# Optimization experiments

Measured on AMD Instinct MI355X. Metric: run time of the kernel, lower is better.

The kernel has to match this reference:

```python
import jax, jax.numpy as jnp
import numpy as np

B, F, D, H = 16384, 39, 16, 2   # batch, fields, embed_dim, heads
VOCAB = 10000                    # per-field vocab
DH = D * H                       # attention output dim per layer (no head split)


def setup_inputs() -> dict:
    key = jax.random.key(0)
    ks = jax.random.split(key, 32)
    def n(k, shape, s=0.05):
        return jax.random.normal(k, shape, jnp.float32) * s
    inp = {"x": jax.random.randint(ks[0], (B, F), 0, VOCAB, dtype=jnp.int32)}
    inp["emb"] = n(ks[1], (F * VOCAB, D))
    idx = 2
    for i, din in enumerate([D, DH, DH]):  # layer0: 16->32, layers 1-2: 32->32
        for nm in ["wq", "wk", "wv", "wr"]:
            inp[f"{nm}{i}"] = n(ks[idx], (din, DH)); idx += 1
    prev = F * DH  # 1248 after flatten
    for i, u in enumerate([128, 64, 32, 1], 1):
        inp[f"w{i}"] = n(ks[idx], (prev, u)); idx += 1
        inp[f"b{i}"] = jnp.zeros((u,), jnp.float32)
        prev = u
    return inp


def reference(x, emb,
              wq0, wk0, wv0, wr0,
              wq1, wk1, wv1, wr1,
              wq2, wk2, wv2, wr2,
              w1, b1, w2, b2, w3, b3, w4, b4):
    offsets = jnp.arange(F, dtype=jnp.int32) * VOCAB
    e = emb[x + offsets]                                   # [B, F, D]
    for wq, wk, wv, wr in [(wq0, wk0, wv0, wr0),
                           (wq1, wk1, wv1, wr1),
                           (wq2, wk2, wv2, wr2)]:
        q = jnp.einsum('bfd,de->bfe', e, wq)               # [B, F, DH]
        k = jnp.einsum('bfd,de->bfe', e, wk)
        v = jnp.einsum('bfd,de->bfe', e, wv)
        att = jax.nn.softmax(jnp.einsum('bfe,bge->bfg', q, k), axis=-1)  # [B,F,F], no scaling
        out = jnp.einsum('bfg,bge->bfe', att, v) + jnp.einsum('bfd,de->bfe', e, wr)
        e = jax.nn.relu(out)
    h = e.reshape(B, F * DH)
    for w, b in [(w1, b1), (w2, b2), (w3, b3)]:
        h = jax.nn.relu(h @ w + b)
    return jax.nn.sigmoid(h @ w4 + b4)                     # [B, 1]
```

## Files before the change

kernel.cpp:

```cpp
#include <hip/hip_runtime.h>
#include <math.h>

#define NF   39
#define NB   16384
#define NVOC 10000

typedef unsigned short u16;
typedef unsigned int   u32;
typedef float f32x4 __attribute__((ext_vector_type(4)));
typedef short s16x8 __attribute__((ext_vector_type(8)));

#define E3_U16   20447232u
#define NSWZ     182272

__device__ __forceinline__ u32 bfadj(float x){
    u32 u = __float_as_uint(x);
    return u + 0x7fffu + ((u >> 16) & 1u);
}
__device__ __forceinline__ u32 pk2(float a, float b){
#if __has_builtin(__builtin_amdgcn_cvt_pk_bf16_f32)
    auto t = __builtin_amdgcn_cvt_pk_bf16_f32(a, b);
    u32 r; __builtin_memcpy(&r, &t, 4); return r;
#else
    return __builtin_amdgcn_perm(bfadj(a), bfadj(b), 0x03020706u);
#endif
}
__device__ __forceinline__ u16 f2bf(float f){ return (u16)(bfadj(f) >> 16); }

__device__ __forceinline__ float fexp2(float x){
#if __has_builtin(__builtin_amdgcn_exp2f)
    return __builtin_amdgcn_exp2f(x);
#else
    return exp2f(x);
#endif
}
__device__ __forceinline__ float frcp(float x){
#if __has_builtin(__builtin_amdgcn_rcpf)
    return __builtin_amdgcn_rcpf(x);
#else
    return 1.f / x;
#endif
}

__device__ __forceinline__ void wave_sync(){
    asm volatile("s_waitcnt lgkmcnt(0)" ::: "memory");
}
__device__ __forceinline__ f32x4 mfma16(s16x8 a, s16x8 b, f32x4 c){
    return __builtin_amdgcn_mfma_f32_16x16x32_bf16(a, b, c, 0, 0, 0);
}
__device__ __forceinline__ void store4(u16* p, f32x4 v){
    *(uint2*)p = make_uint2(pk2(v[0], v[1]), pk2(v[2], v[3]));
}

__global__ void __launch_bounds__(256) swz_kernel(
    const float* __restrict__ wq0, const float* __restrict__ wk0,
    const float* __restrict__ wv0, const float* __restrict__ wr0,
    const float* __restrict__ wq1, const float* __restrict__ wk1,
    const float* __restrict__ wv1, const float* __restrict__ wr1,
    const float* __restrict__ wq2, const float* __restrict__ wk2,
    const float* __restrict__ wv2, const float* __restrict__ wr2,
    const float* __restrict__ w1, const float* __restrict__ w2,
    const float* __restrict__ w3, u16* __restrict__ ws)
{
    int gid = (int)blockIdx.x*256 + (int)threadIdx.x;
    if (gid >= NSWZ) return;
    int w    = gid & 511;
    int lane = w >> 3, j = w & 7;
    int n    = lane & 15, quad = lane >> 4;
    int kin  = quad*8 + j;
    float val;
    if (gid < 12288){
        int mat = gid >> 10;
        int nt  = (gid >> 9) & 1;
        const float* W;
        switch (mat){
            case 0: W = wq0; break; case 1: W = wk0; break;
            case 2: W = wv0; break; case 3: W = wr0; break;
            case 4: W = wq1; break; case 5: W = wk1; break;
            case 6: W = wv1; break; case 7: W = wr1; break;
            case 8: W = wq2; break; case 9: W = wk2; break;
            case 10: W = wv2; break; default: W = wr2; break;
        }
        int din = (mat < 4) ? 16 : 32;
        val = (kin < din) ? W[kin*32 + nt*16 + n] : 0.f;
        if ((mat & 3) == 0) val *= 1.44269504f;
    } else if (gid < 12288 + 159744){
        int tt = (gid - 12288) >> 9;
        int ks = tt >> 3, nt = tt & 7;
        val = w1[(ks*32 + kin)*128 + nt*16 + n];
    } else if (gid < 12288 + 159744 + 8192){
        int tt = (gid - (12288+159744)) >> 9;
        int ks = tt >> 2, nt = tt & 3;
        val = w2[(ks*32 + kin)*64 + nt*16 + n];
    } else {
        int tt = (gid - (12288+159744+8192)) >> 9;
        int ks = tt >> 1, nt = tt & 1;
        val = w3[(ks*32 + kin)*32 + nt*16 + n];
    }
    ws[E3_U16 + gid] = f2bf(val);
}

__global__ void __launch_bounds__(256, 4) attn_kernel(
    const int* __restrict__ x, const float* __restrict__ emb,
    u16* __restrict__ ws)
{
    __shared__ __align__(16) u16 lds[4*5120];
    const int tid  = (int)threadIdx.x;
    const int wid  = tid >> 6, lane = tid & 63;
    const int h    = lane >> 4, nl = lane & 15;
    const int r    = (int)blockIdx.x*4 + wid;

    u16* vBuf = lds + wid*5120;
    u16* eBuf = vBuf;
    u16* kBuf = vBuf + 2048;
    u16* qBuf = kBuf + 1536;
    u16* pBuf = kBuf;
    const u16* wmat = ws + E3_U16;
    const f32x4 z = {0.f, 0.f, 0.f, 0.f};
    const int A_off = nl*8 + (h>>1)*128 + (h&1)*4;

    f32x4 ci;
#pragma unroll
    for (int reg = 0; reg < 4; ++reg)
        ci[reg] = (h*4 + reg >= 7) ? -1e30f : 0.f;

    if (lane < 48){
        int f = lane, mt = f >> 4, fl = f & 15;
        u16* row = eBuf + mt*512 + fl*8;
        if (f < NF){
            const float4* ep = (const float4*)(emb + ((size_t)(x[r*NF + f] + f*NVOC))*16);
            float4 e0 = ep[0], e1 = ep[1], e2 = ep[2], e3 = ep[3];
            *(uint4*)(row)       = make_uint4(pk2(e0.x,e0.y), pk2(e0.z,e0.w),
                                              pk2(e1.x,e1.y), pk2(e1.z,e1.w));
            *(uint4*)(row + 128) = make_uint4(pk2(e2.x,e2.y), pk2(e2.z,e2.w),
                                              pk2(e3.x,e3.y), pk2(e3.z,e3.w));
        } else {
            *(uint4*)(row)       = make_uint4(0,0,0,0);
            *(uint4*)(row + 128) = make_uint4(0,0,0,0);
        }
        *(uint4*)(row + 256) = make_uint4(0,0,0,0);
        *(uint4*)(row + 384) = make_uint4(0,0,0,0);
    }
    wave_sync();

#pragma unroll 1
    for (int L = 0; L < 3; ++L){
        const u16* wB = wmat + L*4096;
        s16x8 bE[3];
#pragma unroll
        for (int nt = 0; nt < 3; ++nt)
            bE[nt] = *(const s16x8*)(eBuf + nt*512 + lane*8);
        wave_sync();

        {
            s16x8 a0 = *(const s16x8*)(wB + lane*8);
            s16x8 a1 = *(const s16x8*)(wB + 512 + lane*8);
#pragma unroll
            for (int nt = 0; nt < 3; ++nt){
                store4(qBuf + nt*512       + A_off, mfma16(a0, bE[nt], z));
                store4(qBuf + nt*512 + 256 + A_off, mfma16(a1, bE[nt], z));
            }
        }
        {
            s16x8 a0 = *(const s16x8*)(wB + 1024 + lane*8);
            s16x8 a1 = *(const s16x8*)(wB + 1536 + lane*8);
#pragma unroll
            for (int nt = 0; nt < 3; ++nt){
                store4(kBuf + nt*512       + A_off, mfma16(a0, bE[nt], z));
                store4(kBuf + nt*512 + 256 + A_off, mfma16(a1, bE[nt], z));
            }
        }
        {
            s16x8 b0 = *(const s16x8*)(wB + 2048 + lane*8);
            s16x8 b1 = *(const s16x8*)(wB + 2560 + lane*8);
#pragma unroll
            for (int mtg = 0; mtg < 3; ++mtg){
                int toff = (mtg>>1)*1024 + (mtg&1)*256;
                store4(vBuf + toff       + A_off, mfma16(bE[mtg], b0, z));
                store4(vBuf + toff + 512 + A_off, mfma16(bE[mtg], b1, z));
            }
            *(uint2*)(vBuf + 2*512 + 256 + lane*4) = make_uint2(0,0);
            *(uint2*)(vBuf + 3*512 + 256 + lane*4) = make_uint2(0,0);
        }
        f32x4 R[2][3];
        {
            s16x8 a0 = *(const s16x8*)(wB + 3072 + lane*8);
            s16x8 a1 = *(const s16x8*)(wB + 3584 + lane*8);
#pragma unroll
            for (int nt = 0; nt < 3; ++nt){
                R[0][nt] = mfma16(a0, bE[nt], z);
                R[1][nt] = mfma16(a1, bE[nt], z);
            }
        }
        wave_sync();

        f32x4 S[3][3];
        {
            s16x8 aK[3], bQ[3];
#pragma unroll
            for (int i = 0; i < 3; ++i){
                aK[i] = *(const s16x8*)(kBuf + i*512 + lane*8);
                bQ[i] = *(const s16x8*)(qBuf + i*512 + lane*8);
            }
#pragma unroll
            for (int mtg = 0; mtg < 3; ++mtg)
#pragma unroll
            for (int nt = 0; nt < 3; ++nt)
                S[mtg][nt] = mfma16(aK[mtg], bQ[nt], (mtg == 2) ? ci : z);
        }
        float inv[3];
#pragma unroll
        for (int nt = 0; nt < 3; ++nt){
            float t = 0.f;
#pragma unroll
            for (int mtg = 0; mtg < 3; ++mtg)
#pragma unroll
            for (int reg = 0; reg < 4; ++reg){
                S[mtg][nt][reg] = fexp2(S[mtg][nt][reg]);
                t += S[mtg][nt][reg];
            }
            t += __shfl_xor(t, 16, 64);
            t += __shfl_xor(t, 32, 64);
            inv[nt] = frcp(t);
        }
#pragma unroll
        for (int mtg = 0; mtg < 3; ++mtg)
#pragma unroll
        for (int nt = 0; nt < 3; ++nt){
            f32x4 p;
#pragma unroll
            for (int reg = 0; reg < 4; ++reg) p[reg] = S[mtg][nt][reg]*inv[nt];
            store4(pBuf + ((mtg>>1)*3 + nt)*512 + (mtg&1)*256 + A_off, p);
        }
        wave_sync();

        s16x8 aV[2][2], bP[2][3];
#pragma unroll
        for (int ks = 0; ks < 2; ++ks){
#pragma unroll
            for (int emt = 0; emt < 2; ++emt)
                aV[ks][emt] = *(const s16x8*)(vBuf + (ks*2+emt)*512 + lane*8);
#pragma unroll
            for (int nt = 0; nt < 3; ++nt)
                bP[ks][nt] = *(const s16x8*)(pBuf + (ks*3+nt)*512 + lane*8);
        }
        wave_sync();
        if (L < 2){
#pragma unroll
            for (int emt = 0; emt < 2; ++emt)
#pragma unroll
            for (int nt = 0; nt < 3; ++nt){
                f32x4 o = mfma16(aV[1][emt], bP[1][nt],
                         mfma16(aV[0][emt], bP[0][nt], R[emt][nt]));
                float m = (nt < 2 || nl < 7) ? 1.f : 0.f;
#pragma unroll
                for (int reg = 0; reg < 4; ++reg)
                    o[reg] = fmaxf(o[reg], 0.f) * m;
                store4(eBuf + nt*512 + emt*256 + A_off, o);
            }
        } else {
            int st = r >> 4, sm = r & 15;
            u32 base = (u32)(st*39)*512u + (u32)(sm*8 + (h>>1)*128 + (h&1)*4);
#pragma unroll
            for (int emt = 0; emt < 2; ++emt)
#pragma unroll
            for (int nt = 0; nt < 3; ++nt){
                f32x4 o = mfma16(aV[1][emt], bP[1][nt],
                         mfma16(aV[0][emt], bP[0][nt], R[emt][nt]));
#pragma unroll
                for (int reg = 0; reg < 4; ++reg)
                    o[reg] = fmaxf(o[reg], 0.f);
                int f = nt*16 + nl;
                if (f < NF)
                    *(uint2*)(ws + base + (u32)f*512u + emt*256) =
                        make_uint2(pk2(o[0], o[1]), pk2(o[2], o[3]));
            }
        }
        wave_sync();
    }
}

__global__ void __launch_bounds__(256, 4) mlp_kernel(
    const float* __restrict__ b1, const float* __restrict__ b2,
    const float* __restrict__ b3, const float* __restrict__ w4,
    const float* __restrict__ b4, const u16* __restrict__ ws,
    float* __restrict__ out)
{
    __shared__ __align__(16) float red[8192];
    __shared__ __align__(16) u16 h1t[2048];
    __shared__ __align__(16) u16 h2t[1024];
    __shared__ float part[32];
    const int tid = (int)threadIdx.x;
    const int w   = tid >> 6, lane = tid & 63;
    const int h   = lane >> 4, nl = lane & 15;
    const int st  = (int)blockIdx.x;
    const int A_off = nl*8 + (h>>1)*128 + (h&1)*4;

    const u16* w1b = ws + E3_U16 + 12288u;
    const u16* w2b = w1b + 159744u;
    const u16* w3b = w2b + 8192u;
    const f32x4 z = {0.f,0.f,0.f,0.f};

    f32x4 acc[8];
#pragma unroll
    for (int nt = 0; nt < 8; ++nt) acc[nt] = z;
#pragma unroll 1
    for (int ks = w; ks < 39; ks += 4){
        s16x8 aE = *(const s16x8*)(ws + (u32)(st*39 + ks)*512u + lane*8);
#pragma unroll
        for (int nt = 0; nt < 8; ++nt){
            s16x8 aW = *(const s16x8*)(w1b + (ks*8 + nt)*512 + lane*8);
            acc[nt] = mfma16(aW, aE, acc[nt]);
        }
    }
#pragma unroll
    for (int nt = 0; nt < 8; ++nt)
        *(f32x4*)(red + (w*8 + nt)*256 + lane*4) = acc[nt];
    __syncthreads();

#pragma unroll
    for (int t = 0; t < 2; ++t){
        int ft = 2*w + t;
        f32x4 s = *(const f32x4*)(red + (0*8 + ft)*256 + lane*4);
#pragma unroll
        for (int p = 1; p < 4; ++p){
            f32x4 q = *(const f32x4*)(red + (p*8 + ft)*256 + lane*4);
#pragma unroll
            for (int reg = 0; reg < 4; ++reg) s[reg] += q[reg];
        }
        float4 bv = *(const float4*)(b1 + ft*16 + h*4);
        f32x4 v;
        v[0] = fmaxf(s[0] + bv.x, 0.f);
        v[1] = fmaxf(s[1] + bv.y, 0.f);
        v[2] = fmaxf(s[2] + bv.z, 0.f);
        v[3] = fmaxf(s[3] + bv.w, 0.f);
        store4(h1t + ft*256 + A_off, v);
    }
    __syncthreads();

    {
        f32x4 a2 = z;
#pragma unroll
        for (int ks = 0; ks < 4; ++ks){
            s16x8 aW = *(const s16x8*)(w2b + (ks*4 + w)*512 + lane*8);
            s16x8 bH = *(const s16x8*)(h1t + ks*512 + lane*8);
            a2 = mfma16(aW, bH, a2);
        }
        float4 bv = *(const float4*)(b2 + w*16 + h*4);
        f32x4 v;
        v[0] = fmaxf(a2[0] + bv.x, 0.f);
        v[1] = fmaxf(a2[1] + bv.y, 0.f);
        v[2] = fmaxf(a2[2] + bv.z, 0.f);
        v[3] = fmaxf(a2[3] + bv.w, 0.f);
        store4(h2t + (w>>1)*512 + (w&1)*256 + A_off, v);
    }
    __syncthreads();

    if (w < 2){
        f32x4 a3 = z;
#pragma unroll
        for (int ks = 0; ks < 2; ++ks){
            s16x8 aW = *(const s16x8*)(w3b + (ks*2 + w)*512 + lane*8);
            s16x8 bH = *(const s16x8*)(h2t + ks*512 + lane*8);
            a3 = mfma16(aW, bH, a3);
        }
        float4 b3v = *(const float4*)(b3 + w*16 + h*4);
        float4 w4v = *(const float4*)(w4 + w*16 + h*4);
        float t = fmaxf(a3[0] + b3v.x, 0.f)*w4v.x
                + fmaxf(a3[1] + b3v.y, 0.f)*w4v.y
                + fmaxf(a3[2] + b3v.z, 0.f)*w4v.z
                + fmaxf(a3[3] + b3v.w, 0.f)*w4v.w;
        t += __shfl_xor(t, 16, 64);
        t += __shfl_xor(t, 32, 64);
        if (h == 0) part[w*16 + nl] = t;
    }
    __syncthreads();
    if (tid < 16){
        float zz = part[tid] + part[16 + tid] + b4[0];
        out[st*16 + tid] = 1.f/(1.f + __expf(-zz));
    }
}

extern "C" void kernel_launch(void* const* d_in, const int* in_sizes, int n_in,
                              void* d_out, int out_size, void* d_ws, size_t ws_size,
                              hipStream_t stream)
{
    (void)in_sizes; (void)n_in; (void)ws_size; (void)out_size;
    const int*   x   = (const int*)d_in[0];
    const float* emb = (const float*)d_in[1];
    u16* ws = (u16*)d_ws;

    swz_kernel<<<(NSWZ+255)/256, 256, 0, stream>>>(
        (const float*)d_in[2],  (const float*)d_in[3],  (const float*)d_in[4],  (const float*)d_in[5],
        (const float*)d_in[6],  (const float*)d_in[7],  (const float*)d_in[8],  (const float*)d_in[9],
        (const float*)d_in[10], (const float*)d_in[11], (const float*)d_in[12], (const float*)d_in[13],
        (const float*)d_in[14], (const float*)d_in[16], (const float*)d_in[18], ws);

    attn_kernel<<<NB/4, 256, 0, stream>>>(x, emb, ws);

    mlp_kernel<<<NB/16, 256, 0, stream>>>(
        (const float*)d_in[15], (const float*)d_in[17], (const float*)d_in[19],
        (const float*)d_in[20], (const float*)d_in[21], ws, (float*)d_out);
}
```

Measured before the change: 189.6 us.

## Process two samples per wave in attention kernel and defer softmax normalization

Each wave now handles two batch rows, sharing the weight fragment loads across both and interleaving their MFMA chains, with the block size reduced to 128 threads. Softmax normalization moves out of the probability store into the output epilogue as a fused multiply-add with the residual, and the residual is no longer seeded into the MFMA accumulator. A redundant per-layer zeroing of the V padding is hoisted into the prologue, and the MLP K loop is unrolled by two. This doubles register pressure per wave, which may lower occupancy.

```diff
diff --git a/kernel.cpp b/kernel.cpp
--- a/kernel.cpp
+++ b/kernel.cpp
@@ -100,21 +100,19 @@
     ws[E3_U16 + gid] = f2bf(val);
 }
 
-__global__ void __launch_bounds__(256, 4) attn_kernel(
+__global__ void __launch_bounds__(128, 2) attn_kernel(
     const int* __restrict__ x, const float* __restrict__ emb,
     u16* __restrict__ ws)
 {
-    __shared__ __align__(16) u16 lds[4*5120];
+    __shared__ __align__(16) u16 lds[2*2*5120];
     const int tid  = (int)threadIdx.x;
     const int wid  = tid >> 6, lane = tid & 63;
     const int h    = lane >> 4, nl = lane & 15;
-    const int r    = (int)blockIdx.x*4 + wid;
-
-    u16* vBuf = lds + wid*5120;
-    u16* eBuf = vBuf;
-    u16* kBuf = vBuf + 2048;
-    u16* qBuf = kBuf + 1536;
-    u16* pBuf = kBuf;
+    const int r0   = (int)blockIdx.x*4 + wid*2;
+
+    u16* base[2];
+    base[0] = lds + wid*10240;
+    base[1] = base[0] + 5120;
     const u16* wmat = ws + E3_U16;
     const f32x4 z = {0.f, 0.f, 0.f, 0.f};
     const int A_off = nl*8 + (h>>1)*128 + (h&1)*4;
@@ -124,78 +122,101 @@
     for (int reg = 0; reg < 4; ++reg)
         ci[reg] = (h*4 + reg >= 7) ? -1e30f : 0.f;
 
-    if (lane < 48){
-        int f = lane, mt = f >> 4, fl = f & 15;
-        u16* row = eBuf + mt*512 + fl*8;
-        if (f < NF){
-            const float4* ep = (const float4*)(emb + ((size_t)(x[r*NF + f] + f*NVOC))*16);
-            float4 e0 = ep[0], e1 = ep[1], e2 = ep[2], e3 = ep[3];
-            *(uint4*)(row)       = make_uint4(pk2(e0.x,e0.y), pk2(e0.z,e0.w),
-                                              pk2(e1.x,e1.y), pk2(e1.z,e1.w));
-            *(uint4*)(row + 128) = make_uint4(pk2(e2.x,e2.y), pk2(e2.z,e2.w),
-                                              pk2(e3.x,e3.y), pk2(e3.z,e3.w));
-        } else {
-            *(uint4*)(row)       = make_uint4(0,0,0,0);
-            *(uint4*)(row + 128) = make_uint4(0,0,0,0);
-        }
-        *(uint4*)(row + 256) = make_uint4(0,0,0,0);
-        *(uint4*)(row + 384) = make_uint4(0,0,0,0);
+#pragma unroll
+    for (int s = 0; s < 2; ++s){
+        u16* eBuf = base[s];
+        if (lane < 48){
+            int f = lane, mt = f >> 4, fl = f & 15;
+            u16* row = eBuf + mt*512 + fl*8;
+            if (f < NF){
+                const float4* ep = (const float4*)(emb + ((size_t)(x[(r0+s)*NF + f] + f*NVOC))*16);
+                float4 e0 = ep[0], e1 = ep[1], e2 = ep[2], e3 = ep[3];
+                *(uint4*)(row)       = make_uint4(pk2(e0.x,e0.y), pk2(e0.z,e0.w),
+                                                  pk2(e1.x,e1.y), pk2(e1.z,e1.w));
+                *(uint4*)(row + 128) = make_uint4(pk2(e2.x,e2.y), pk2(e2.z,e2.w),
+                                                  pk2(e3.x,e3.y), pk2(e3.z,e3.w));
+            } else {
+                *(uint4*)(row)       = make_uint4(0,0,0,0);
+                *(uint4*)(row + 128) = make_uint4(0,0,0,0);
+            }
+            *(uint4*)(row + 256) = make_uint4(0,0,0,0);
+            *(uint4*)(row + 384) = make_uint4(0,0,0,0);
+        }
+        *(uint2*)(base[s] + 3*512 + 256 + lane*4) = make_uint2(0,0);
     }
     wave_sync();
 
 #pragma unroll 1
     for (int L = 0; L < 3; ++L){
         const u16* wB = wmat + L*4096;
-        s16x8 bE[3];
+        s16x8 bE[2][3];
+#pragma unroll
+        for (int s = 0; s < 2; ++s)
 #pragma unroll
         for (int nt = 0; nt < 3; ++nt)
-            bE[nt] = *(const s16x8*)(eBuf + nt*512 + lane*8);
+            bE[s][nt] = *(const s16x8*)(base[s] + nt*512 + lane*8);
         wave_sync();
 
         {
             s16x8 a0 = *(const s16x8*)(wB + lane*8);
             s16x8 a1 = *(const s16x8*)(wB + 512 + lane*8);
 #pragma unroll
-            for (int nt = 0; nt < 3; ++nt){
-                store4(qBuf + nt*512       + A_off, mfma16(a0, bE[nt], z));
-                store4(qBuf + nt*512 + 256 + A_off, mfma16(a1, bE[nt], z));
+            for (int s = 0; s < 2; ++s){
+                u16* qBuf = base[s] + 2048 + 1536;
+#pragma unroll
+                for (int nt = 0; nt < 3; ++nt){
+                    store4(qBuf + nt*512       + A_off, mfma16(a0, bE[s][nt], z));
+                    store4(qBuf + nt*512 + 256 + A_off, mfma16(a1, bE[s][nt], z));
+                }
             }
         }
         {
             s16x8 a0 = *(const s16x8*)(wB + 1024 + lane*8);
             s16x8 a1 = *(const s16x8*)(wB + 1536 + lane*8);
 #pragma unroll
-            for (int nt = 0; nt < 3; ++nt){
-                store4(kBuf + nt*512       + A_off, mfma16(a0, bE[nt], z));
-                store4(kBuf + nt*512 + 256 + A_off, mfma16(a1, bE[nt], z));
+            for (int s = 0; s < 2; ++s){
+                u16* kBuf = base[s] + 2048;
+#pragma unroll
+                for (int nt = 0; nt < 3; ++nt){
+                    store4(kBuf + nt*512       + A_off, mfma16(a0, bE[s][nt], z));
+                    store4(kBuf + nt*512 + 256 + A_off, mfma16(a1, bE[s][nt], z));
+                }
             }
         }
         {
             s16x8 b0 = *(const s16x8*)(wB + 2048 + lane*8);
             s16x8 b1 = *(const s16x8*)(wB + 2560 + lane*8);
 #pragma unroll
-            for (int mtg = 0; mtg < 3; ++mtg){
-                int toff = (mtg>>1)*1024 + (mtg&1)*256;
-                store4(vBuf + toff       + A_off, mfma16(bE[mtg], b0, z));
-                store4(vBuf + toff + 512 + A_off, mfma16(bE[mtg], b1, z));
-            }
-            *(uint2*)(vBuf + 2*512 + 256 + lane*4) = make_uint2(0,0);
-            *(uint2*)(vBuf + 3*512 + 256 + lane*4) = make_uint2(0,0);
-        }
-        f32x4 R[2][3];
+            for (int s = 0; s < 2; ++s){
+                u16* vBuf = base[s];
+#pragma unroll
+                for (int mtg = 0; mtg < 3; ++mtg){
+                    int toff = (mtg>>1)*1024 + (mtg&1)*256;
+                    store4(vBuf + toff       + A_off, mfma16(bE[s][mtg], b0, z));
+                    store4(vBuf + toff + 512 + A_off, mfma16(bE[s][mtg], b1, z));
+                }
+                *(uint2*)(vBuf + 2*512 + 256 + lane*4) = make_uint2(0,0);
+            }
+        }
+        f32x4 R[2][2][3];
         {
             s16x8 a0 = *(const s16x8*)(wB + 3072 + lane*8);
             s16x8 a1 = *(const s16x8*)(wB + 3584 + lane*8);
 #pragma unroll
+            for (int s = 0; s < 2; ++s)
+#pragma unroll
             for (int nt = 0; nt < 3; ++nt){
-                R[0][nt] = mfma16(a0, bE[nt], z);
-                R[1][nt] = mfma16(a1, bE[nt], z);
+                R[s][0][nt] = mfma16(a0, bE[s][nt], z);
+                R[s][1][nt] = mfma16(a1, bE[s][nt], z);
             }
         }
         wave_sync();
 
-        f32x4 S[3][3];
-        {
+        f32x4 S[2][3][3];
+#pragma unroll
+        for (int s = 0; s < 2; ++s){
+            u16* kBuf = base[s] + 2048;
+            u16* qBuf = kBuf + 1536;
             s16x8 aK[3], bQ[3];
 #pragma unroll
             for (int i = 0; i < 3; ++i){
@@ -206,9 +227,11 @@
             for (int mtg = 0; mtg < 3; ++mtg)
 #pragma unroll
             for (int nt = 0; nt < 3; ++nt)
-                S[mtg][nt] = mfma16(aK[mtg], bQ[nt], (mtg == 2) ? ci : z);
-        }
-        float inv[3];
+                S[s][mtg][nt] = mfma16(aK[mtg], bQ[nt], (mtg == 2) ? ci : z);
+        }
+        float inv[2][3];
+#pragma unroll
+        for (int s = 0; s < 2; ++s)
 #pragma unroll
         for (int nt = 0; nt < 3; ++nt){
             float t = 0.f;
@@ -216,64 +239,71 @@
             for (int mtg = 0; mtg < 3; ++mtg)
 #pragma unroll
             for (int reg = 0; reg < 4; ++reg){
-                S[mtg][nt][reg] = fexp2(S[mtg][nt][reg]);
-                t += S[mtg][nt][reg];
+                S[s][mtg][nt][reg] = fexp2(S[s][mtg][nt][reg]);
+                t += S[s][mtg][nt][reg];
             }
             t += __shfl_xor(t, 16, 64);
             t += __shfl_xor(t, 32, 64);
-            inv[nt] = frcp(t);
-        }
-#pragma unroll
-        for (int mtg = 0; mtg < 3; ++mtg)
-#pragma unroll
-        for (int nt = 0; nt < 3; ++nt){
-            f32x4 p;
-#pragma unroll
-            for (int reg = 0; reg < 4; ++reg) p[reg] = S[mtg][nt][reg]*inv[nt];
-            store4(pBuf + ((mtg>>1)*3 + nt)*512 + (mtg&1)*256 + A_off, p);
+            inv[s][nt] = frcp(t);
+        }
+#pragma unroll
+        for (int s = 0; s < 2; ++s){
+            u16* pBuf = base[s] + 2048;
+#pragma unroll
+            for (int mtg = 0; mtg < 3; ++mtg)
+#pragma unroll
+            for (int nt = 0; nt < 3; ++nt)
+                store4(pBuf + ((mtg>>1)*3 + nt)*512 + (mtg&1)*256 + A_off,
+                       S[s][mtg][nt]);
         }
         wave_sync();
 
-        s16x8 aV[2][2], bP[2][3];
-#pragma unroll
-        for (int ks = 0; ks < 2; ++ks){
-#pragma unroll
-            for (int emt = 0; emt < 2; ++emt)
-                aV[ks][emt] = *(const s16x8*)(vBuf + (ks*2+emt)*512 + lane*8);
-#pragma unroll
-            for (int nt = 0; nt < 3; ++nt)
-                bP[ks][nt] = *(const s16x8*)(pBuf + (ks*3+nt)*512 + lane*8);
-        }
-        wave_sync();
-        if (L < 2){
-#pragma unroll
-            for (int emt = 0; emt < 2; ++emt)
-#pragma unroll
-            for (int nt = 0; nt < 3; ++nt){
-                f32x4 o = mfma16(aV[1][emt], bP[1][nt],
-                         mfma16(aV[0][emt], bP[0][nt], R[emt][nt]));
-                float m = (nt < 2 || nl < 7) ? 1.f : 0.f;
-#pragma unroll
-                for (int reg = 0; reg < 4; ++reg)
-                    o[reg] = fmaxf(o[reg], 0.f) * m;
-                store4(eBuf + nt*512 + emt*256 + A_off, o);
-            }
-        } else {
-            int st = r >> 4, sm = r & 15;
-            u32 base = (u32)(st*39)*512u + (u32)(sm*8 + (h>>1)*128 + (h&1)*4);
-#pragma unroll
-            for (int emt = 0; emt < 2; ++emt)
-#pragma unroll
-            for (int nt = 0; nt < 3; ++nt){
-                f32x4 o = mfma16(aV[1][emt], bP[1][nt],
-                         mfma16(aV[0][emt], bP[0][nt], R[emt][nt]));
-#pragma unroll
-                for (int reg = 0; reg < 4; ++reg)
-                    o[reg] = fmaxf(o[reg], 0.f);
-                int f = nt*16 + nl;
-                if (f < NF)
-                    *(uint2*)(ws + base + (u32)f*512u + emt*256) =
-                        make_uint2(pk2(o[0], o[1]), pk2(o[2], o[3]));
+#pragma unroll
+        for (int s = 0; s < 2; ++s){
+            u16* vBuf = base[s];
+            u16* pBuf = base[s] + 2048;
+            s16x8 aV[2][2], bP[2][3];
+#pragma unroll
+            for (int ks = 0; ks < 2; ++ks){
+#pragma unroll
+                for (int emt = 0; emt < 2; ++emt)
+                    aV[ks][emt] = *(const s16x8*)(vBuf + (ks*2+emt)*512 + lane*8);
+#pragma unroll
+                for (int nt = 0; nt < 3; ++nt)
+                    bP[ks][nt] = *(const s16x8*)(pBuf + (ks*3+nt)*512 + lane*8);
+            }
+            wave_sync();
+            if (L < 2){
+#pragma unroll
+                for (int emt = 0; emt < 2; ++emt)
+#pragma unroll
+                for (int nt = 0; nt < 3; ++nt){
+                    f32x4 o = mfma16(aV[1][emt], bP[1][nt],
+                             mfma16(aV[0][emt], bP[0][nt], z));
+                    float m = (nt < 2 || nl < 7) ? 1.f : 0.f;
+#pragma unroll
+                    for (int reg = 0; reg < 4; ++reg)
+                        o[reg] = fmaxf(fmaf(o[reg], inv[s][nt], R[s][emt][nt][reg]), 0.f) * m;
+                    store4(base[s] + nt*512 + emt*256 + A_off, o);
+                }
+            } else {
+                int rr = r0 + s;
+                int st = rr >> 4, sm = rr & 15;
+                u32 gbase = (u32)(st*39)*512u + (u32)(sm*8 + (h>>1)*128 + (h&1)*4);
+#pragma unroll
+                for (int emt = 0; emt < 2; ++emt)
+#pragma unroll
+                for (int nt = 0; nt < 3; ++nt){
+                    f32x4 o = mfma16(aV[1][emt], bP[1][nt],
+                             mfma16(aV[0][emt], bP[0][nt], z));
+#pragma unroll
+                    for (int reg = 0; reg < 4; ++reg)
+                        o[reg] = fmaxf(fmaf(o[reg], inv[s][nt], R[s][emt][nt][reg]), 0.f);
+                    int f = nt*16 + nl;
+                    if (f < NF)
+                        *(uint2*)(ws + gbase + (u32)f*512u + emt*256) =
+                            make_uint2(pk2(o[0], o[1]), pk2(o[2], o[3]));
+                }
             }
         }
         wave_sync();
@@ -304,7 +334,7 @@
     f32x4 acc[8];
 #pragma unroll
     for (int nt = 0; nt < 8; ++nt) acc[nt] = z;
-#pragma unroll 1
+#pragma unroll 2
     for (int ks = w; ks < 39; ks += 4){
         s16x8 aE = *(const s16x8*)(ws + (u32)(st*39 + ks)*512u + lane*8);
 #pragma unroll
@@ -396,7 +426,7 @@
         (const float*)d_in[10], (const float*)d_in[11], (const float*)d_in[12], (const float*)d_in[13],
         (const float*)d_in[14], (const float*)d_in[16], (const float*)d_in[18], ws);
 
-    attn_kernel<<<NB/4, 256, 0, stream>>>(x, emb, ws);
+    attn_kernel<<<NB/4, 128, 0, stream>>>(x, emb, ws);
 
     mlp_kernel<<<NB/16, 256, 0, stream>>>(
         (const float*)d_in[15], (const float*)d_in[17], (const float*)d_in[19],
```

After: 204.2 us. 7.7% more time.
